# Performance work log

Hardware: AMD Instinct MI355X
Metric: run time of the kernel (lower is better)

Reference implementation:

```python
import jax, jax.numpy as jnp
import numpy as np

NUM_HEADS = 16


def setup_inputs() -> dict:
    key = jax.random.key(0)
    ks = jax.random.split(key, 6)
    B, S, D = 2, 2048, 1024
    x = jax.random.normal(ks[0], (B, S, D), dtype=jnp.float32)
    # Linear weights stored as [d_in, d_out] so forward is x @ W (qkv_bias=False)
    scale = 1.0 / np.sqrt(D)
    Wq = jax.random.normal(ks[1], (D, D), dtype=jnp.float32) * scale
    Wk = jax.random.normal(ks[2], (D, D), dtype=jnp.float32) * scale
    Wv = jax.random.normal(ks[3], (D, D), dtype=jnp.float32) * scale
    Wo = jax.random.normal(ks[4], (D, D), dtype=jnp.float32) * scale
    bo = jax.random.normal(ks[5], (D,), dtype=jnp.float32) * 0.01
    return {"x": x, "Wq": Wq, "Wk": Wk, "Wv": Wv, "Wo": Wo, "bo": bo}


def reference(x, Wq, Wk, Wv, Wo, bo):
    B, S, D = x.shape
    H = NUM_HEADS
    hd = D // H

    def split_heads(t):  # [B,S,D] -> [B,H,S,hd]
        return t.reshape(B, S, H, hd).transpose(0, 2, 1, 3)

    q = split_heads(x @ Wq)
    k = split_heads(x @ Wk)
    v = split_heads(x @ Wv)

    # full score matrix [B,H,S,S]
    scores = jnp.einsum('bhsd,bhtd->bhst', q, k)
    causal = jnp.triu(jnp.ones((S, S), dtype=bool), k=1)
    scores = jnp.where(causal, -jnp.inf, scores)
    attn = jax.nn.softmax(scores * (hd ** -0.5), axis=-1)
    # dropout p=0.0 -> identity
    out = jnp.einsum('bhst,bhtd->bhsd', attn, v)
    out = out.transpose(0, 2, 1, 3).reshape(B, S, D)
    return out @ Wo + bo
```

## Files before the change

kernel.cpp:

```cpp
#include <hip/hip_runtime.h>

typedef unsigned short ushort_t;
typedef unsigned int uint_t;
typedef __attribute__((ext_vector_type(8))) short short8;
typedef __attribute__((ext_vector_type(4))) float floatx4;

#define S_LEN 2048
#define D_DIM 1024
#define H_NUM 16
#define HD 64
#define GBUF (128 * 32)

__device__ __forceinline__ float bf2f(ushort_t u) {
    union { uint_t i; float f; } c; c.i = ((uint_t)u) << 16; return c.f;
}
__device__ __forceinline__ ushort_t f2bf(float f) {
    union { float f; uint_t i; } c; c.f = f;
    uint_t r = c.i + 0x7fffu + ((c.i >> 16) & 1u);
    return (ushort_t)(r >> 16);
}
__device__ __forceinline__ uint_t cvtpk_bf16(float lo, float hi) {
    uint_t d;
    asm("v_cvt_pk_bf16_f32 %0, %1, %2" : "=v"(d) : "v"(lo), "v"(hi));
    return d;
}

__device__ __forceinline__ void g2l16(const ushort_t* g, ushort_t* l) {
    __builtin_amdgcn_global_load_lds(
        (const __attribute__((address_space(1))) void*)g,
        (__attribute__((address_space(3))) void*)l, 16, 0, 0);
}

__global__ __launch_bounds__(256, 4) void cast_x_kernel(
        const float* __restrict__ in, ushort_t* __restrict__ out) {
    const int idx = (blockIdx.x * 256 + threadIdx.x) * 4;
    const float4 v = *(const float4*)(in + idx);
    ushort4 o;
    o.x = f2bf(v.x); o.y = f2bf(v.y); o.z = f2bf(v.z); o.w = f2bf(v.w);
    *(ushort4*)(out + idx) = o;
}

__global__ __launch_bounds__(256, 2) void transpose4_kernel(
        const float* __restrict__ W0, const float* __restrict__ W1,
        const float* __restrict__ W2, const float* __restrict__ W3,
        ushort_t* __restrict__ T0, ushort_t* __restrict__ T1,
        ushort_t* __restrict__ T2, ushort_t* __restrict__ T3) {
    const int z = blockIdx.z;
    const float* in  = (z == 0) ? W0 : (z == 1) ? W1 : (z == 2) ? W2 : W3;
    ushort_t*    out = (z == 0) ? T0 : (z == 1) ? T1 : (z == 2) ? T2 : T3;
    __shared__ __align__(16) ushort_t t[64][65];
    const int r0 = blockIdx.y * 64, c0 = blockIdx.x * 64;
    const int tr = threadIdx.x >> 4;
    const int tc = (threadIdx.x & 15) * 4;
#pragma unroll
    for (int i = 0; i < 4; ++i) {
        const int row = tr + i * 16;
        const float4 v = *(const float4*)(in + (size_t)(r0 + row) * D_DIM + c0 + tc);
        t[row][tc + 0] = f2bf(v.x); t[row][tc + 1] = f2bf(v.y);
        t[row][tc + 2] = f2bf(v.z); t[row][tc + 3] = f2bf(v.w);
    }
    __syncthreads();
#pragma unroll
    for (int i = 0; i < 4; ++i) {
        const int n = tr + i * 16;
        ushort4 v;
        v.x = t[tc + 0][n]; v.y = t[tc + 1][n];
        v.z = t[tc + 2][n]; v.w = t[tc + 3][n];
        *(ushort4*)(out + (size_t)(c0 + n) * D_DIM + r0 + tc) = v;
    }
}

__device__ __forceinline__ void gemm_tile(
        const ushort_t* __restrict__ A, const ushort_t* __restrict__ BT,
        const int m0, const int n0,
        ushort_t* As, ushort_t* Bs, floatx4 acc[4][4]) {
    const int tid  = threadIdx.x;
    const int w    = tid >> 6;
    const int wm   = (w >> 1) * 64;
    const int wn   = (w & 1) * 64;
    const int lrow = tid & 15;
    const int kq   = ((tid & 63) >> 4) * 8;

    const int flat0 = tid * 8;
    const int flat1 = (256 + tid) * 8;
    const int row0 = flat0 >> 5, kk0 = flat0 & 31;
    const int row1 = flat1 >> 5, kk1 = flat1 & 31;

    const ushort_t* ga0 = A  + (size_t)(m0 + row0) * D_DIM + kk0;
    const ushort_t* gb0 = BT + (size_t)(n0 + row0) * D_DIM + kk0;
    const ushort_t* ga1 = A  + (size_t)(m0 + row1) * D_DIM + kk1;
    const ushort_t* gb1 = BT + (size_t)(n0 + row1) * D_DIM + kk1;

    const int nsteps = D_DIM / 32;

    g2l16(ga0, As + flat0);
    g2l16(gb0, Bs + flat0);
    g2l16(ga1, As + flat1);
    g2l16(gb1, Bs + flat1);
    g2l16(ga0 + 32, As + GBUF + flat0);
    g2l16(gb0 + 32, Bs + GBUF + flat0);
    g2l16(ga1 + 32, As + GBUF + flat1);
    g2l16(gb1 + 32, Bs + GBUF + flat1);

    int cur = 0;
    for (int k = 0; k < nsteps; ++k) {
        if (k == nsteps - 1)
            asm volatile("s_waitcnt vmcnt(0) lgkmcnt(0)" ::: "memory");
        else
            asm volatile("s_waitcnt vmcnt(4) lgkmcnt(0)" ::: "memory");
        __builtin_amdgcn_sched_barrier(0);
        __builtin_amdgcn_s_barrier();

        const ushort_t* Ac = As + cur * GBUF;
        const ushort_t* Bc = Bs + cur * GBUF;
        short8 av[4], bv[4];
#pragma unroll
        for (int i = 0; i < 4; ++i)
            av[i] = *(const short8*)(Ac + (wm + i * 16 + lrow) * 32 + kq);
#pragma unroll
        for (int j = 0; j < 4; ++j)
            bv[j] = *(const short8*)(Bc + (wn + j * 16 + lrow) * 32 + kq);

        if (k + 2 < nsteps) {
            const int nb = (cur + 2 >= 3) ? cur - 1 : cur + 2;
            ushort_t* An = As + nb * GBUF;
            ushort_t* Bn = Bs + nb * GBUF;
            const int ko = (k + 2) * 32;
            g2l16(ga0 + ko, An + flat0);
            g2l16(gb0 + ko, Bn + flat0);
            g2l16(ga1 + ko, An + flat1);
            g2l16(gb1 + ko, Bn + flat1);
        }

#pragma unroll
        for (int i = 0; i < 4; ++i)
#pragma unroll
            for (int j = 0; j < 4; ++j)
                acc[i][j] = __builtin_amdgcn_mfma_f32_16x16x32_bf16(
                    av[i], bv[j], acc[i][j], 0, 0, 0);

        cur = (cur + 1 >= 3) ? 0 : cur + 1;
    }
}

__global__ __launch_bounds__(256, 3) void gemm_qkv_kernel(
        const ushort_t* __restrict__ A,
        const ushort_t* __restrict__ WqT, const ushort_t* __restrict__ WkT,
        const ushort_t* __restrict__ WvT,
        ushort_t* __restrict__ Qo, ushort_t* __restrict__ Ko,
        ushort_t* __restrict__ Vo) {
    const ushort_t* BT = (blockIdx.z == 0) ? WqT : (blockIdx.z == 1) ? WkT : WvT;
    ushort_t* C        = (blockIdx.z == 0) ? Qo  : (blockIdx.z == 1) ? Ko  : Vo;
    const float sc     = (blockIdx.z == 0) ? 0.18033688f : 1.0f;
    __shared__ __align__(16) ushort_t As[3 * GBUF];
    __shared__ __align__(16) ushort_t Bs[3 * GBUF];
    const int m0 = blockIdx.y * 128, n0 = blockIdx.x * 128;

    floatx4 acc[4][4] = {};
    gemm_tile(A, BT, m0, n0, As, Bs, acc);

    const int tid = threadIdx.x;
    const int w = tid >> 6, wm = (w >> 1) * 64, wn = (w & 1) * 64;
    const int lrow = tid & 15;
    const int rquad = ((tid & 63) >> 4) * 4;
#pragma unroll
    for (int i = 0; i < 4; ++i) {
        const int mbase = m0 + wm + i * 16 + rquad;
#pragma unroll
        for (int j = 0; j < 4; ++j) {
            const int gn = n0 + wn + j * 16 + lrow;
#pragma unroll
            for (int r = 0; r < 4; ++r)
                C[(size_t)(mbase + r) * D_DIM + gn] = f2bf(acc[i][j][r] * sc);
        }
    }
}

__global__ __launch_bounds__(256, 2) void gemm_out_kernel(
        const ushort_t* __restrict__ A, const ushort_t* __restrict__ WoT,
        const float* __restrict__ bias, float* __restrict__ C) {
    __shared__ __align__(16) ushort_t As[3 * GBUF];
    __shared__ __align__(16) ushort_t Bs[3 * GBUF];
    const int m0 = blockIdx.y * 128, n0 = blockIdx.x * 128;

    floatx4 acc[4][4] = {};
    gemm_tile(A, WoT, m0, n0, As, Bs, acc);

    const int tid = threadIdx.x;
    const int w = tid >> 6, wm = (w >> 1) * 64, wn = (w & 1) * 64;
    const int lrow = tid & 15;
    const int rquad = ((tid & 63) >> 4) * 4;
#pragma unroll
    for (int i = 0; i < 4; ++i) {
        const int mbase = m0 + wm + i * 16 + rquad;
#pragma unroll
        for (int j = 0; j < 4; ++j) {
            const int gn = n0 + wn + j * 16 + lrow;
            const float badd = bias[gn];
#pragma unroll
            for (int r = 0; r < 4; ++r)
                C[(size_t)(mbase + r) * D_DIM + gn] = acc[i][j][r] + badd;
        }
    }
}

__global__ __launch_bounds__(256, 4) void attn_mfma_kernel(
        const ushort_t* __restrict__ Q, const ushort_t* __restrict__ K,
        const ushort_t* __restrict__ V, ushort_t* __restrict__ O) {
    __shared__ __align__(16) ushort_t Ks[64 * 64];
    __shared__ __align__(16) ushort_t Vt[64 * 64];

    const int bh  = blockIdx.x;
    const int b   = bh >> 4, h = bh & 15;
    const int g   = blockIdx.y & 7;
    const int p   = blockIdx.y >> 3;
    const int qt  = (p == 0) ? g : (p == 1) ? (15 - g)
                  : (p == 2) ? (16 + g) : (31 - g);
    const int q0  = qt * 64;
    const int tid = threadIdx.x;
    const int wq  = tid >> 6;
    const int lane = tid & 63;
    const int col  = lane & 15;
    const int quad = lane >> 4;
    const int c7 = col & 7;
    const int qw0  = q0 + wq * 16;
    const size_t rowbase = (size_t)b * S_LEN;
    const int ch0 = h * HD;
    const int q4 = quad * 4;
    const int gbase = (lane & 48) << 2;

    const int skey = tid >> 2;
    const int schk = tid & 3;
    const int vkp = tid & 31;
    const int vdc = tid >> 5;

    short8 aq[2];
#pragma unroll
    for (int kc = 0; kc < 2; ++kc)
        aq[kc] = *(const short8*)(Q + (rowbase + qw0 + col) * D_DIM
                                    + ch0 + kc * 32 + quad * 8);

    floatx4 oacc[4] = {};
    float mrun0 = -1e30f, lrun0 = 0.0f;

    const int ntiles = qt + 1;

    short8 krA, krB, vrA, vrB;
    {
        const ushort_t* kg = K + (rowbase + skey) * D_DIM + ch0 + schk * 16;
        krA = *(const short8*)(kg);
        krB = *(const short8*)(kg + 8);
        const ushort_t* vg = V + (rowbase + 2 * vkp) * D_DIM + ch0 + vdc * 8;
        vrA = *(const short8*)(vg);
        vrB = *(const short8*)(vg + D_DIM);
    }

    for (int t = 0; t < ntiles; ++t) {
        const int kb = t * 64;
        __syncthreads();
        {
            const int sw = skey & 7;
            *(short8*)(Ks + skey * 64 + (((2 * schk) ^ sw) << 3)) = krA;
            *(short8*)(Ks + skey * 64 + (((2 * schk + 1) ^ sw) << 3)) = krB;
        }
#pragma unroll
        for (int e = 0; e < 8; ++e) {
            const int d = vdc * 8 + e;
            const uint_t pkv = (uint_t)(ushort_t)vrA[e] | ((uint_t)(ushort_t)vrB[e] << 16);
            *(uint_t*)(Vt + d * 64 + ((2 * vkp) ^ ((d & 7) << 3))) = pkv;
        }
        {
            const int kbn = (t + 1 < ntiles) ? (t + 1) * 64 : 0;
            const ushort_t* kg = K + (rowbase + kbn + skey) * D_DIM + ch0 + schk * 16;
            krA = *(const short8*)(kg);
            krB = *(const short8*)(kg + 8);
            const ushort_t* vg = V + (rowbase + kbn + 2 * vkp) * D_DIM + ch0 + vdc * 8;
            vrA = *(const short8*)(vg);
            vrB = *(const short8*)(vg + D_DIM);
        }
        __syncthreads();

        if (kb <= qw0 + 15) {
            floatx4 sa[4] = {};
            __builtin_amdgcn_s_setprio(1);
#pragma unroll
            for (int kc = 0; kc < 2; ++kc)
#pragma unroll
                for (int j = 0; j < 4; ++j) {
                    const short8 bk = *(const short8*)(
                        Ks + (j * 16 + col) * 64 + (((kc * 4 + quad) ^ c7) << 3));
                    sa[j] = __builtin_amdgcn_mfma_f32_16x16x32_bf16(
                        bk, aq[kc], sa[j], 0, 0, 0);
                }
            __builtin_amdgcn_s_setprio(0);

            const bool needmask = (kb + 63 > qw0);
            if (needmask) {
                const int qrow = qw0 + col;
#pragma unroll
                for (int j = 0; j < 4; ++j)
#pragma unroll
                    for (int r = 0; r < 4; ++r)
                        if (kb + j * 16 + q4 + r > qrow) sa[j][r] = -1e30f;
            }
            float mx = sa[0][0];
#pragma unroll
            for (int j = 0; j < 4; ++j)
#pragma unroll
                for (int r = 0; r < 4; ++r) mx = fmaxf(mx, sa[j][r]);
            mx = fmaxf(mx, __shfl_xor(mx, 16));
            mx = fmaxf(mx, __shfl_xor(mx, 32));
            const float mn = fmaxf(mrun0, mx);
            const float al = __builtin_amdgcn_exp2f(mrun0 - mn);
            mrun0 = mn;
            float rs = 0.0f;
#pragma unroll
            for (int j = 0; j < 4; ++j)
#pragma unroll
                for (int r = 0; r < 4; ++r) {
                    const float p2 = __builtin_amdgcn_exp2f(sa[j][r] - mn);
                    sa[j][r] = p2;
                    rs += p2;
                }
            lrun0 = lrun0 * al + rs;
            float al4[4];
#pragma unroll
            for (int r = 0; r < 4; ++r)
                al4[r] = __int_as_float(__builtin_amdgcn_ds_bpermute(
                    gbase + ((q4 + r) << 2), __float_as_int(al)));
#pragma unroll
            for (int jd = 0; jd < 4; ++jd)
#pragma unroll
                for (int r = 0; r < 4; ++r) oacc[jd][r] *= al4[r];
            uint_t pk[4][2];
#pragma unroll
            for (int j = 0; j < 4; ++j) {
                pk[j][0] = cvtpk_bf16(sa[j][0], sa[j][1]);
                pk[j][1] = cvtpk_bf16(sa[j][2], sa[j][3]);
            }
            const int aLo = (col + ((quad & 1) << 5)) << 2;
            const int aHi = aLo + 64;
            uint_t res[4][2][2];
#pragma unroll
            for (int j = 0; j < 4; ++j)
#pragma unroll
                for (int p2 = 0; p2 < 2; ++p2) {
                    res[j][p2][0] = (uint_t)__builtin_amdgcn_ds_bpermute(aLo, (int)pk[j][p2]);
                    res[j][p2][1] = (uint_t)__builtin_amdgcn_ds_bpermute(aHi, (int)pk[j][p2]);
                }
            const bool b5 = (quad >> 1) != 0;
            union { short8 s; uint_t u[4]; } ap[2];
#pragma unroll
            for (int kc = 0; kc < 2; ++kc)
#pragma unroll
                for (int d = 0; d < 4; ++d)
                    ap[kc].u[d] = b5 ? res[2 * kc + 1][d & 1][d >> 1]
                                     : res[2 * kc][d & 1][d >> 1];
            __builtin_amdgcn_s_setprio(1);
#pragma unroll
            for (int kc = 0; kc < 2; ++kc)
#pragma unroll
                for (int jd = 0; jd < 4; ++jd) {
                    const short8 bv = *(const short8*)(
                        Vt + (jd * 16 + col) * 64 + (((kc * 4 + quad) ^ c7) << 3));
                    oacc[jd] = __builtin_amdgcn_mfma_f32_16x16x32_bf16(
                        ap[kc].s, bv, oacc[jd], 0, 0, 0);
                }
            __builtin_amdgcn_s_setprio(0);
        }
    }

    float l = lrun0;
    l += __shfl_xor(l, 16);
    l += __shfl_xor(l, 32);
#pragma unroll
    for (int r = 0; r < 4; ++r) {
        const float lr = __int_as_float(__builtin_amdgcn_ds_bpermute(
            gbase + ((q4 + r) << 2), __float_as_int(l)));
        const float inv = 1.0f / lr;
        const int row = qw0 + q4 + r;
#pragma unroll
        for (int jd = 0; jd < 4; ++jd)
            O[(rowbase + row) * D_DIM + ch0 + jd * 16 + col] =
                f2bf(oacc[jd][r] * inv);
    }
}

extern "C" void kernel_launch(void* const* d_in, const int* in_sizes, int n_in,
                              void* d_out, int out_size, void* d_ws, size_t ws_size,
                              hipStream_t stream) {
    const float* x  = (const float*)d_in[0];
    const float* Wq = (const float*)d_in[1];
    const float* Wk = (const float*)d_in[2];
    const float* Wv = (const float*)d_in[3];
    const float* Wo = (const float*)d_in[4];
    const float* bo = (const float*)d_in[5];
    float* out = (float*)d_out;

    char* ws = (char*)d_ws;
    const size_t MB = 1024 * 1024;
    ushort_t* xb  = (ushort_t*)(ws + 0 * MB);
    ushort_t* WqT = (ushort_t*)(ws + 8 * MB);
    ushort_t* WkT = (ushort_t*)(ws + 10 * MB);
    ushort_t* WvT = (ushort_t*)(ws + 12 * MB);
    ushort_t* WoT = (ushort_t*)(ws + 14 * MB);
    ushort_t* Qb  = (ushort_t*)(ws + 16 * MB);
    ushort_t* Kb  = (ushort_t*)(ws + 24 * MB);
    ushort_t* Vb  = (ushort_t*)(ws + 32 * MB);
    ushort_t* Ob  = (ushort_t*)(ws + 40 * MB);

    cast_x_kernel<<<4096, 256, 0, stream>>>(x, xb);
    transpose4_kernel<<<dim3(16, 16, 4), 256, 0, stream>>>(
        Wq, Wk, Wv, Wo, WqT, WkT, WvT, WoT);

    gemm_qkv_kernel<<<dim3(8, 32, 3), 256, 0, stream>>>(
        xb, WqT, WkT, WvT, Qb, Kb, Vb);

    attn_mfma_kernel<<<dim3(32, 32), 256, 0, stream>>>(Qb, Kb, Vb, Ob);

    gemm_out_kernel<<<dim3(8, 32), 256, 0, stream>>>(Ob, WoT, bo, out);
}
```

Before: 187.9 us.

## Enlarge attention query tile to 128 rows with two 16-row groups per wave

Each attention block now handles 128 query rows instead of 64, and each wave processes two 16-row query groups against every K/V tile staged in shared memory. This halves the number of K/V tile loads and LDS staging passes per query row. In exchange, register pressure roughly doubles for the accumulators, so launch bounds drop to 2 blocks per SM. The grid is halved to 512 blocks with a simpler causal load-balancing pairing.

```diff
diff --git a/kernel.cpp b/kernel.cpp
--- a/kernel.cpp
+++ b/kernel.cpp
@@ -204,7 +204,7 @@
     }
 }
 
-__global__ __launch_bounds__(256, 4) void attn_mfma_kernel(
+__global__ __launch_bounds__(256, 2) void attn_mfma_kernel(
         const ushort_t* __restrict__ Q, const ushort_t* __restrict__ K,
         const ushort_t* __restrict__ V, ushort_t* __restrict__ O) {
     __shared__ __align__(16) ushort_t Ks[64 * 64];
@@ -212,18 +212,17 @@
 
     const int bh  = blockIdx.x;
     const int b   = bh >> 4, h = bh & 15;
-    const int g   = blockIdx.y & 7;
-    const int p   = blockIdx.y >> 3;
-    const int qt  = (p == 0) ? g : (p == 1) ? (15 - g)
-                  : (p == 2) ? (16 + g) : (31 - g);
-    const int q0  = qt * 64;
+    const int gy  = blockIdx.y & 7;
+    const int py  = blockIdx.y >> 3;
+    const int qt  = py ? (15 - gy) : gy;
+    const int q0  = qt * 128;
     const int tid = threadIdx.x;
     const int wq  = tid >> 6;
     const int lane = tid & 63;
     const int col  = lane & 15;
     const int quad = lane >> 4;
     const int c7 = col & 7;
-    const int qw0  = q0 + wq * 16;
+    const int qw0  = q0 + wq * 32;
     const size_t rowbase = (size_t)b * S_LEN;
     const int ch0 = h * HD;
     const int q4 = quad * 4;
@@ -234,16 +233,19 @@
     const int vkp = tid & 31;
     const int vdc = tid >> 5;
 
-    short8 aq[2];
-#pragma unroll
-    for (int kc = 0; kc < 2; ++kc)
-        aq[kc] = *(const short8*)(Q + (rowbase + qw0 + col) * D_DIM
-                                    + ch0 + kc * 32 + quad * 8);
-
-    floatx4 oacc[4] = {};
-    float mrun0 = -1e30f, lrun0 = 0.0f;
-
-    const int ntiles = qt + 1;
+    short8 aq[2][2];
+#pragma unroll
+    for (int gq = 0; gq < 2; ++gq)
+#pragma unroll
+        for (int kc = 0; kc < 2; ++kc)
+            aq[gq][kc] = *(const short8*)(Q + (rowbase + qw0 + gq * 16 + col) * D_DIM
+                                            + ch0 + kc * 32 + quad * 8);
+
+    floatx4 oacc[2][4] = {};
+    float mrun[2] = {-1e30f, -1e30f};
+    float lrun[2] = {0.0f, 0.0f};
+
+    const int ntiles = 2 * qt + 2;
 
     short8 krA, krB, vrA, vrB;
     {
@@ -280,109 +282,117 @@
         }
         __syncthreads();
 
-        if (kb <= qw0 + 15) {
-            floatx4 sa[4] = {};
-            __builtin_amdgcn_s_setprio(1);
-#pragma unroll
-            for (int kc = 0; kc < 2; ++kc)
+        if (kb <= qw0 + 31) {
+#pragma unroll
+            for (int gq = 0; gq < 2; ++gq) {
+                if (kb > qw0 + gq * 16 + 15) continue;
+                const int grow0 = qw0 + gq * 16;
+                floatx4 sa[4] = {};
+                __builtin_amdgcn_s_setprio(1);
+#pragma unroll
+                for (int kc = 0; kc < 2; ++kc)
+#pragma unroll
+                    for (int j = 0; j < 4; ++j) {
+                        const short8 bk = *(const short8*)(
+                            Ks + (j * 16 + col) * 64 + (((kc * 4 + quad) ^ c7) << 3));
+                        sa[j] = __builtin_amdgcn_mfma_f32_16x16x32_bf16(
+                            bk, aq[gq][kc], sa[j], 0, 0, 0);
+                    }
+                __builtin_amdgcn_s_setprio(0);
+
+                const bool needmask = (kb + 63 > grow0);
+                if (needmask) {
+                    const int qrow = grow0 + col;
+#pragma unroll
+                    for (int j = 0; j < 4; ++j)
+#pragma unroll
+                        for (int r = 0; r < 4; ++r)
+                            if (kb + j * 16 + q4 + r > qrow) sa[j][r] = -1e30f;
+                }
+                float mx = sa[0][0];
+#pragma unroll
+                for (int j = 0; j < 4; ++j)
+#pragma unroll
+                    for (int r = 0; r < 4; ++r) mx = fmaxf(mx, sa[j][r]);
+                mx = fmaxf(mx, __shfl_xor(mx, 16));
+                mx = fmaxf(mx, __shfl_xor(mx, 32));
+                const float mn = fmaxf(mrun[gq], mx);
+                const float al = __builtin_amdgcn_exp2f(mrun[gq] - mn);
+                mrun[gq] = mn;
+                float rs = 0.0f;
+#pragma unroll
+                for (int j = 0; j < 4; ++j)
+#pragma unroll
+                    for (int r = 0; r < 4; ++r) {
+                        const float p2 = __builtin_amdgcn_exp2f(sa[j][r] - mn);
+                        sa[j][r] = p2;
+                        rs += p2;
+                    }
+                lrun[gq] = lrun[gq] * al + rs;
+                float al4[4];
+#pragma unroll
+                for (int r = 0; r < 4; ++r)
+                    al4[r] = __int_as_float(__builtin_amdgcn_ds_bpermute(
+                        gbase + ((q4 + r) << 2), __float_as_int(al)));
+#pragma unroll
+                for (int jd = 0; jd < 4; ++jd)
+#pragma unroll
+                    for (int r = 0; r < 4; ++r) oacc[gq][jd][r] *= al4[r];
+                uint_t pk[4][2];
 #pragma unroll
                 for (int j = 0; j < 4; ++j) {
-                    const short8 bk = *(const short8*)(
-                        Ks + (j * 16 + col) * 64 + (((kc * 4 + quad) ^ c7) << 3));
-                    sa[j] = __builtin_amdgcn_mfma_f32_16x16x32_bf16(
-                        bk, aq[kc], sa[j], 0, 0, 0);
+                    pk[j][0] = cvtpk_bf16(sa[j][0], sa[j][1]);
+                    pk[j][1] = cvtpk_bf16(sa[j][2], sa[j][3]);
                 }
-            __builtin_amdgcn_s_setprio(0);
-
-            const bool needmask = (kb + 63 > qw0);
-            if (needmask) {
-                const int qrow = qw0 + col;
+                const int aLo = (col + ((quad & 1) << 5)) << 2;
+                const int aHi = aLo + 64;
+                uint_t res[4][2][2];
 #pragma unroll
                 for (int j = 0; j < 4; ++j)
 #pragma unroll
-                    for (int r = 0; r < 4; ++r)
-                        if (kb + j * 16 + q4 + r > qrow) sa[j][r] = -1e30f;
+                    for (int p2 = 0; p2 < 2; ++p2) {
+                        res[j][p2][0] = (uint_t)__builtin_amdgcn_ds_bpermute(aLo, (int)pk[j][p2]);
+                        res[j][p2][1] = (uint_t)__builtin_amdgcn_ds_bpermute(aHi, (int)pk[j][p2]);
+                    }
+                const bool b5 = (quad >> 1) != 0;
+                union { short8 s; uint_t u[4]; } ap[2];
+#pragma unroll
+                for (int kc = 0; kc < 2; ++kc)
+#pragma unroll
+                    for (int d = 0; d < 4; ++d)
+                        ap[kc].u[d] = b5 ? res[2 * kc + 1][d & 1][d >> 1]
+                                         : res[2 * kc][d & 1][d >> 1];
+                __builtin_amdgcn_s_setprio(1);
+#pragma unroll
+                for (int kc = 0; kc < 2; ++kc)
+#pragma unroll
+                    for (int jd = 0; jd < 4; ++jd) {
+                        const short8 bv = *(const short8*)(
+                            Vt + (jd * 16 + col) * 64 + (((kc * 4 + quad) ^ c7) << 3));
+                        oacc[gq][jd] = __builtin_amdgcn_mfma_f32_16x16x32_bf16(
+                            ap[kc].s, bv, oacc[gq][jd], 0, 0, 0);
+                    }
+                __builtin_amdgcn_s_setprio(0);
             }
-            float mx = sa[0][0];
-#pragma unroll
-            for (int j = 0; j < 4; ++j)
-#pragma unroll
-                for (int r = 0; r < 4; ++r) mx = fmaxf(mx, sa[j][r]);
-            mx = fmaxf(mx, __shfl_xor(mx, 16));
-            mx = fmaxf(mx, __shfl_xor(mx, 32));
-            const float mn = fmaxf(mrun0, mx);
-            const float al = __builtin_amdgcn_exp2f(mrun0 - mn);
-            mrun0 = mn;
-            float rs = 0.0f;
-#pragma unroll
-            for (int j = 0; j < 4; ++j)
-#pragma unroll
-                for (int r = 0; r < 4; ++r) {
-                    const float p2 = __builtin_amdgcn_exp2f(sa[j][r] - mn);
-                    sa[j][r] = p2;
-                    rs += p2;
-                }
-            lrun0 = lrun0 * al + rs;
-            float al4[4];
-#pragma unroll
-            for (int r = 0; r < 4; ++r)
-                al4[r] = __int_as_float(__builtin_amdgcn_ds_bpermute(
-                    gbase + ((q4 + r) << 2), __float_as_int(al)));
+        }
+    }
+
+#pragma unroll
+    for (int gq = 0; gq < 2; ++gq) {
+        float l = lrun[gq];
+        l += __shfl_xor(l, 16);
+        l += __shfl_xor(l, 32);
+#pragma unroll
+        for (int r = 0; r < 4; ++r) {
+            const float lr = __int_as_float(__builtin_amdgcn_ds_bpermute(
+                gbase + ((q4 + r) << 2), __float_as_int(l)));
+            const float inv = 1.0f / lr;
+            const int row = qw0 + gq * 16 + q4 + r;
 #pragma unroll
             for (int jd = 0; jd < 4; ++jd)
-#pragma unroll
-                for (int r = 0; r < 4; ++r) oacc[jd][r] *= al4[r];
-            uint_t pk[4][2];
-#pragma unroll
-            for (int j = 0; j < 4; ++j) {
-                pk[j][0] = cvtpk_bf16(sa[j][0], sa[j][1]);
-                pk[j][1] = cvtpk_bf16(sa[j][2], sa[j][3]);
-            }
-            const int aLo = (col + ((quad & 1) << 5)) << 2;
-            const int aHi = aLo + 64;
-            uint_t res[4][2][2];
-#pragma unroll
-            for (int j = 0; j < 4; ++j)
-#pragma unroll
-                for (int p2 = 0; p2 < 2; ++p2) {
-                    res[j][p2][0] = (uint_t)__builtin_amdgcn_ds_bpermute(aLo, (int)pk[j][p2]);
-                    res[j][p2][1] = (uint_t)__builtin_amdgcn_ds_bpermute(aHi, (int)pk[j][p2]);
-                }
-            const bool b5 = (quad >> 1) != 0;
-            union { short8 s; uint_t u[4]; } ap[2];
-#pragma unroll
-            for (int kc = 0; kc < 2; ++kc)
-#pragma unroll
-                for (int d = 0; d < 4; ++d)
-                    ap[kc].u[d] = b5 ? res[2 * kc + 1][d & 1][d >> 1]
-                                     : res[2 * kc][d & 1][d >> 1];
-            __builtin_amdgcn_s_setprio(1);
-#pragma unroll
-            for (int kc = 0; kc < 2; ++kc)
-#pragma unroll
-                for (int jd = 0; jd < 4; ++jd) {
-                    const short8 bv = *(const short8*)(
-                        Vt + (jd * 16 + col) * 64 + (((kc * 4 + quad) ^ c7) << 3));
-                    oacc[jd] = __builtin_amdgcn_mfma_f32_16x16x32_bf16(
-                        ap[kc].s, bv, oacc[jd], 0, 0, 0);
-                }
-            __builtin_amdgcn_s_setprio(0);
-        }
-    }
-
-    float l = lrun0;
-    l += __shfl_xor(l, 16);
-    l += __shfl_xor(l, 32);
-#pragma unroll
-    for (int r = 0; r < 4; ++r) {
-        const float lr = __int_as_float(__builtin_amdgcn_ds_bpermute(
-            gbase + ((q4 + r) << 2), __float_as_int(l)));
-        const float inv = 1.0f / lr;
-        const int row = qw0 + q4 + r;
-#pragma unroll
-        for (int jd = 0; jd < 4; ++jd)
-            O[(rowbase + row) * D_DIM + ch0 + jd * 16 + col] =
-                f2bf(oacc[jd][r] * inv);
+                O[(rowbase + row) * D_DIM + ch0 + jd * 16 + col] =
+                    f2bf(oacc[gq][jd][r] * inv);
+        }
     }
 }
 
@@ -416,7 +426,7 @@
     gemm_qkv_kernel<<<dim3(8, 32, 3), 256, 0, stream>>>(
         xb, WqT, WkT, WvT, Qb, Kb, Vb);
 
-    attn_mfma_kernel<<<dim3(32, 32), 256, 0, stream>>>(Qb, Kb, Vb, Ob);
+    attn_mfma_kernel<<<dim3(32, 16), 256, 0, stream>>>(Qb, Kb, Vb, Ob);
 
     gemm_out_kernel<<<dim3(8, 32), 256, 0, stream>>>(Ob, WoT, bo, out);
 }
```

Result: slower. 199.2 us (+6.0%).

## Load K fragments directly from global memory into registers, dropping K LDS staging

Applied to the files above, without the earlier changes.

The attention kernel stops staging K tiles through shared memory. Each wave now loads its MFMA B-operand fragments for the current key tile straight from global memory into registers, and skips that load when the tile is fully masked. This removes the LDS writes and reads for K and shrinks shared memory use. In exchange, each of the four waves fetches the same K tile separately, which quadruples global and L2 traffic for K. The K load is also no longer prefetched one tile ahead, so its latency falls on the critical path right before the MFMAs.

```diff
diff --git a/kernel.cpp b/kernel.cpp
--- a/kernel.cpp
+++ b/kernel.cpp
@@ -207,7 +207,6 @@
 __global__ __launch_bounds__(256, 4) void attn_mfma_kernel(
         const ushort_t* __restrict__ Q, const ushort_t* __restrict__ K,
         const ushort_t* __restrict__ V, ushort_t* __restrict__ O) {
-    __shared__ __align__(16) ushort_t Ks[64 * 64];
     __shared__ __align__(16) ushort_t Vt[64 * 64];
 
     const int bh  = blockIdx.x;
@@ -229,8 +228,6 @@
     const int q4 = quad * 4;
     const int gbase = (lane & 48) << 2;
 
-    const int skey = tid >> 2;
-    const int schk = tid & 3;
     const int vkp = tid & 31;
     const int vdc = tid >> 5;
 
@@ -240,16 +237,15 @@
         aq[kc] = *(const short8*)(Q + (rowbase + qw0 + col) * D_DIM
                                     + ch0 + kc * 32 + quad * 8);
 
+    const ushort_t* kfb = K + (rowbase + col) * D_DIM + ch0 + quad * 8;
+
     floatx4 oacc[4] = {};
     float mrun0 = -1e30f, lrun0 = 0.0f;
 
     const int ntiles = qt + 1;
 
-    short8 krA, krB, vrA, vrB;
+    short8 vrA, vrB;
     {
-        const ushort_t* kg = K + (rowbase + skey) * D_DIM + ch0 + schk * 16;
-        krA = *(const short8*)(kg);
-        krB = *(const short8*)(kg + 8);
         const ushort_t* vg = V + (rowbase + 2 * vkp) * D_DIM + ch0 + vdc * 8;
         vrA = *(const short8*)(vg);
         vrB = *(const short8*)(vg + D_DIM);
@@ -257,12 +253,8 @@
 
     for (int t = 0; t < ntiles; ++t) {
         const int kb = t * 64;
+        const bool active = (kb <= qw0 + 15);
         __syncthreads();
-        {
-            const int sw = skey & 7;
-            *(short8*)(Ks + skey * 64 + (((2 * schk) ^ sw) << 3)) = krA;
-            *(short8*)(Ks + skey * 64 + (((2 * schk + 1) ^ sw) << 3)) = krB;
-        }
 #pragma unroll
         for (int e = 0; e < 8; ++e) {
             const int d = vdc * 8 + e;
@@ -271,27 +263,30 @@
         }
         {
             const int kbn = (t + 1 < ntiles) ? (t + 1) * 64 : 0;
-            const ushort_t* kg = K + (rowbase + kbn + skey) * D_DIM + ch0 + schk * 16;
-            krA = *(const short8*)(kg);
-            krB = *(const short8*)(kg + 8);
             const ushort_t* vg = V + (rowbase + kbn + 2 * vkp) * D_DIM + ch0 + vdc * 8;
             vrA = *(const short8*)(vg);
             vrB = *(const short8*)(vg + D_DIM);
         }
+        short8 kf[2][4];
+        if (active) {
+            const ushort_t* kt = kfb + (size_t)kb * D_DIM;
+#pragma unroll
+            for (int kc = 0; kc < 2; ++kc)
+#pragma unroll
+                for (int j = 0; j < 4; ++j)
+                    kf[kc][j] = *(const short8*)(kt + (size_t)(j * 16) * D_DIM + kc * 32);
+        }
         __syncthreads();
 
-        if (kb <= qw0 + 15) {
+        if (active) {
             floatx4 sa[4] = {};
             __builtin_amdgcn_s_setprio(1);
 #pragma unroll
             for (int kc = 0; kc < 2; ++kc)
 #pragma unroll
-                for (int j = 0; j < 4; ++j) {
-                    const short8 bk = *(const short8*)(
-                        Ks + (j * 16 + col) * 64 + (((kc * 4 + quad) ^ c7) << 3));
+                for (int j = 0; j < 4; ++j)
                     sa[j] = __builtin_amdgcn_mfma_f32_16x16x32_bf16(
-                        bk, aq[kc], sa[j], 0, 0, 0);
-                }
+                        kf[kc][j], aq[kc], sa[j], 0, 0, 0);
             __builtin_amdgcn_s_setprio(0);
 
             const bool needmask = (kb + 63 > qw0);
```

After: 232.7 us. +23.9%, slower.
